# Kernel tuning notes

Measured on AMD Instinct MI355X. Metric: run time of the kernel, lower is better.

Reference implementation:

```python
import jax, jax.numpy as jnp
import numpy as np

DIM = 768
HQ = 8
HKV = 2
HD = 64
B = 1
S = 4096


def setup_inputs() -> dict:
    key = jax.random.key(0)
    ks = jax.random.split(key, 9)
    s = 0.02
    return {
        "x": jax.random.normal(ks[0], (B, S, DIM), jnp.float32),
        "Wq": jax.random.normal(ks[1], (DIM, HQ * HD), jnp.float32) * s,
        "bq": jax.random.normal(ks[2], (HQ * HD,), jnp.float32) * s,
        "Wk": jax.random.normal(ks[3], (DIM, HKV * HD), jnp.float32) * s,
        "bk": jax.random.normal(ks[4], (HKV * HD,), jnp.float32) * s,
        "Wv": jax.random.normal(ks[5], (DIM, HKV * HD), jnp.float32) * s,
        "bv": jax.random.normal(ks[6], (HKV * HD,), jnp.float32) * s,
        "Wo": jax.random.normal(ks[7], (HQ * HD, DIM), jnp.float32) * s,
        "bo": jax.random.normal(ks[8], (DIM,), jnp.float32) * s,
    }


def reference(x, Wq, bq, Wk, bk, Wv, bv, Wo, bo):
    bsz, q_len, _ = x.shape
    n_rep = HQ // HKV
    # projections
    q = (x @ Wq + bq).reshape(bsz, q_len, HQ, HD).transpose(0, 2, 1, 3)   # [b,hq,s,d]
    k = (x @ Wk + bk).reshape(bsz, q_len, HKV, HD).transpose(0, 2, 1, 3)  # [b,hkv,s,d]
    v = (x @ Wv + bv).reshape(bsz, q_len, HKV, HD).transpose(0, 2, 1, 3)
    # repeat_kv: expand kv heads to match query heads
    k = jnp.broadcast_to(k[:, :, None], (bsz, HKV, n_rep, q_len, HD)).reshape(bsz, HQ, q_len, HD)
    v = jnp.broadcast_to(v[:, :, None], (bsz, HKV, n_rep, q_len, HD)).reshape(bsz, HQ, q_len, HD)
    # full materialized attention (no mask in the original)
    att = jnp.einsum("bhqd,bhkd->bhqk", q, k) / jnp.sqrt(jnp.float32(HD))
    att = jax.nn.softmax(att.astype(jnp.float32), axis=-1).astype(q.dtype)  # [b,hq,s,s]
    out = jnp.einsum("bhqk,bhkd->bhqd", att, v)
    out = out.transpose(0, 2, 1, 3).reshape(bsz, q_len, HQ * HD)
    out = out @ Wo + bo
    return (out, att)
```

## Files before the change

### kernel.cpp

```cpp
#include <hip/hip_runtime.h>
#include <hip/hip_bf16.h>


#define DIM   768
#define Sc    4096

typedef __bf16 bfrag __attribute__((ext_vector_type(8)));
typedef float  facc  __attribute__((ext_vector_type(4)));

#define MFMA_BF16(a,b,c) __builtin_amdgcn_mfma_f32_16x16x32_bf16((a),(b),(c),0,0,0)

__global__ __launch_bounds__(256) void prep_kernel(
    const float* __restrict__ x,  const float* __restrict__ Wq,
    const float* __restrict__ Wk, const float* __restrict__ Wv,
    const float* __restrict__ Wo,
    __bf16* __restrict__ xb, __bf16* __restrict__ WqkvT, __bf16* __restrict__ WobT)
{
  int i = blockIdx.x * 256 + threadIdx.x;
  const int NX = Sc * DIM;
  const int NW = DIM * DIM;
  if (i < NX) { xb[i] = (__bf16)x[i]; return; }
  i -= NX;
  if (i < NW) {
    int n = i / DIM, c = i - n * DIM;
    float v;
    if (n < 512)      v = Wq[c * 512 + n];
    else if (n < 640) v = Wk[c * 128 + (n - 512)];
    else              v = Wv[c * 128 + (n - 640)];
    WqkvT[i] = (__bf16)v;
    return;
  }
  i -= NW;
  {
    int n = i / 512, k = i - n * 512;
    WobT[i] = (__bf16)Wo[k * DIM + n];
  }
}

template<int MODE>
__global__ __launch_bounds__(256) void gemm_kernel(
    const __bf16* __restrict__ A, const __bf16* __restrict__ BT, int Kd,
    const float* __restrict__ b0, const float* __restrict__ b1, const float* __restrict__ b2,
    __bf16* __restrict__ Qb, __bf16* __restrict__ Kb, __bf16* __restrict__ VTb,
    float* __restrict__ Cout)
{
  const int tid  = threadIdx.x;
  const int w    = tid >> 6;
  const int lane = tid & 63;
  const int i16  = lane & 15;
  const int quad = lane >> 4;
  const int n0   = blockIdx.x * 64;
  const int m0   = blockIdx.y * 64;

  __shared__ __attribute__((aligned(16))) __bf16 Al[64 * 72];
  __shared__ __attribute__((aligned(16))) __bf16 Bl[64 * 72];

  facc acc[4];
#pragma unroll
  for (int nt = 0; nt < 4; ++nt) acc[nt] = (facc){0.f, 0.f, 0.f, 0.f};

  const int nkt = Kd >> 6;
  for (int kt = 0; kt < nkt; ++kt) {
#pragma unroll
    for (int it = 0; it < 2; ++it) {
      int idx = tid + it * 256;
      int r = idx >> 3, ch = idx & 7;
      *(uint4*)&Al[r * 72 + ch * 8] =
          *(const uint4*)(A + (size_t)(m0 + r) * Kd + (kt * 64 + ch * 8));
    }
#pragma unroll
    for (int it = 0; it < 2; ++it) {
      int idx = tid + it * 256;
      int r = idx >> 3, ch = idx & 7;
      *(uint4*)&Bl[r * 72 + ch * 8] =
          *(const uint4*)(BT + (size_t)(n0 + r) * Kd + (kt * 64 + ch * 8));
    }
    __syncthreads();
#pragma unroll
    for (int ks = 0; ks < 2; ++ks) {
      bfrag a = *(const bfrag*)&Al[(w * 16 + i16) * 72 + ks * 32 + quad * 8];
#pragma unroll
      for (int nt = 0; nt < 4; ++nt) {
        bfrag b = *(const bfrag*)&Bl[(nt * 16 + i16) * 72 + ks * 32 + quad * 8];
        acc[nt] = MFMA_BF16(a, b, acc[nt]);
      }
    }
    __syncthreads();
  }

#pragma unroll
  for (int nt = 0; nt < 4; ++nt) {
    const int n = n0 + nt * 16 + i16;
    const int rbase = m0 + w * 16 + quad * 4;
    if (MODE == 0) {
      float bias;
      if (n < 512)      bias = b0[n];
      else if (n < 640) bias = b1[n - 512];
      else              bias = b2[n - 640];
#pragma unroll
      for (int reg = 0; reg < 4; ++reg) {
        float v = acc[nt][reg] + bias;
        int row = rbase + reg;
        if (n < 512) {
          int hh = n >> 6, d = n & 63;
          Qb[((size_t)hh * Sc + row) * 64 + d] = (__bf16)(v * 0.125f);
        } else if (n < 640) {
          int hh = (n - 512) >> 6, d = n & 63;
          Kb[((size_t)hh * Sc + row) * 64 + d] = (__bf16)v;
        } else {
          int hh = (n - 640) >> 6, d = n & 63;
          VTb[(size_t)hh * 64 * Sc + (size_t)d * Sc + row] = (__bf16)v;
        }
      }
    } else {
      float bias = b0[n];
#pragma unroll
      for (int reg = 0; reg < 4; ++reg)
        Cout[(size_t)(rbase + reg) * DIM + n] = acc[nt][reg] + bias;
    }
  }
}

#define PFSTRIDE 68
#define PFWAVE   (16 * PFSTRIDE + 4)

__global__ __launch_bounds__(256, 6) void attn_kernel(
    const __bf16* __restrict__ Qb, const __bf16* __restrict__ Kb,
    const __bf16* __restrict__ VTb,
    float* __restrict__ att, __bf16* __restrict__ OAb)
{
  const int tid  = threadIdx.x;
  const int w    = tid >> 6;
  const int lane = tid & 63;
  const int i16  = lane & 15;
  const int quad = lane >> 4;
  const int h    = blockIdx.y;
  const int kvh  = h >> 2;
  const int q0   = blockIdx.x * 16;

  __shared__ __attribute__((aligned(16))) float Pf[4 * PFWAVE];
  __shared__ float SM[4][16], SL[4][16];

  const __bf16* Kbase = Kb  + (size_t)kvh * Sc * 64;
  const __bf16* Vbase = VTb + (size_t)kvh * 64 * Sc;

  bfrag qf[2];
#pragma unroll
  for (int ks = 0; ks < 2; ++ks)
    qf[ks] = *(const bfrag*)(Qb + ((size_t)h * Sc + q0 + i16) * 64 + ks * 32 + quad * 8);

  float mrun[4], lrun[4];
#pragma unroll
  for (int r = 0; r < 4; ++r) { mrun[r] = -1e30f; lrun[r] = 0.f; }

  const int key0 = w * 1024;

  for (int kt = 0; kt < 16; ++kt) {
    const int kb0 = key0 + kt * 64;
    facc s[4];
#pragma unroll
    for (int nt = 0; nt < 4; ++nt) s[nt] = (facc){0.f, 0.f, 0.f, 0.f};
#pragma unroll
    for (int ks = 0; ks < 2; ++ks)
#pragma unroll
      for (int nt = 0; nt < 4; ++nt) {
        bfrag kf = *(const bfrag*)(Kbase + (size_t)(kb0 + nt * 16 + i16) * 64 + ks * 32 + quad * 8);
        s[nt] = MFMA_BF16(qf[ks], kf, s[nt]);
      }
#pragma unroll
    for (int r = 0; r < 4; ++r) {
      float tm = fmaxf(fmaxf(s[0][r], s[1][r]), fmaxf(s[2][r], s[3][r]));
      tm = fmaxf(tm, __shfl_xor(tm, 1));
      tm = fmaxf(tm, __shfl_xor(tm, 2));
      tm = fmaxf(tm, __shfl_xor(tm, 4));
      tm = fmaxf(tm, __shfl_xor(tm, 8));
      float mnew = fmaxf(mrun[r], tm);
      float ts = __expf(s[0][r] - mnew) + __expf(s[1][r] - mnew)
               + __expf(s[2][r] - mnew) + __expf(s[3][r] - mnew);
      ts += __shfl_xor(ts, 1);
      ts += __shfl_xor(ts, 2);
      ts += __shfl_xor(ts, 4);
      ts += __shfl_xor(ts, 8);
      lrun[r] = lrun[r] * __expf(mrun[r] - mnew) + ts;
      mrun[r] = mnew;
    }
  }

  if (i16 == 0) {
#pragma unroll
    for (int r = 0; r < 4; ++r) { SM[w][quad * 4 + r] = mrun[r]; SL[w][quad * 4 + r] = lrun[r]; }
  }
  __syncthreads();
  float mglob[4], linv[4];
#pragma unroll
  for (int r = 0; r < 4; ++r) {
    const int rr = quad * 4 + r;
    float m0v = SM[0][rr], m1v = SM[1][rr], m2v = SM[2][rr], m3v = SM[3][rr];
    float mg = fmaxf(fmaxf(m0v, m1v), fmaxf(m2v, m3v));
    float lg = SL[0][rr] * __expf(m0v - mg) + SL[1][rr] * __expf(m1v - mg)
             + SL[2][rr] * __expf(m2v - mg) + SL[3][rr] * __expf(m3v - mg);
    mglob[r] = mg;
    linv[r]  = 1.f / lg;
  }

  facc oacc[4];
#pragma unroll
  for (int nt = 0; nt < 4; ++nt) oacc[nt] = (facc){0.f, 0.f, 0.f, 0.f};

  float* attb = att + (size_t)h * Sc * Sc;
  float* Pw   = Pf + w * PFWAVE;

  for (int kt = 0; kt < 16; ++kt) {
    const int kb0 = key0 + kt * 64;
    facc s[4];
#pragma unroll
    for (int nt = 0; nt < 4; ++nt) s[nt] = (facc){0.f, 0.f, 0.f, 0.f};
#pragma unroll
    for (int ks = 0; ks < 2; ++ks)
#pragma unroll
      for (int nt = 0; nt < 4; ++nt) {
        bfrag kf = *(const bfrag*)(Kbase + (size_t)(kb0 + nt * 16 + i16) * 64 + ks * 32 + quad * 8);
        s[nt] = MFMA_BF16(qf[ks], kf, s[nt]);
      }
#pragma unroll
    for (int nt = 0; nt < 4; ++nt)
#pragma unroll
      for (int r = 0; r < 4; ++r)
        Pw[(quad * 4 + r) * PFSTRIDE + nt * 16 + i16] =
            __expf(s[nt][r] - mglob[r]) * linv[r];
    bfrag pa[2];
#pragma unroll
    for (int ks = 0; ks < 2; ++ks) {
      facc p0 = *(const facc*)&Pw[i16 * PFSTRIDE + ks * 32 + quad * 8];
      facc p1 = *(const facc*)&Pw[i16 * PFSTRIDE + ks * 32 + quad * 8 + 4];
      bfrag t;
      t[0] = (__bf16)p0[0]; t[1] = (__bf16)p0[1]; t[2] = (__bf16)p0[2]; t[3] = (__bf16)p0[3];
      t[4] = (__bf16)p1[0]; t[5] = (__bf16)p1[1]; t[6] = (__bf16)p1[2]; t[7] = (__bf16)p1[3];
      pa[ks] = t;
    }
#pragma unroll
    for (int ks = 0; ks < 2; ++ks)
#pragma unroll
      for (int nt = 0; nt < 4; ++nt) {
        bfrag vf = *(const bfrag*)(Vbase + (size_t)(nt * 16 + i16) * Sc + kb0 + ks * 32 + quad * 8);
        oacc[nt] = MFMA_BF16(pa[ks], vf, oacc[nt]);
      }
#pragma unroll
    for (int it = 0; it < 4; ++it) {
      int flat = it * 64 + lane;
      int row = flat >> 4, c4 = flat & 15;
      facc v = *(const facc*)&Pw[row * PFSTRIDE + c4 * 4];
      *(facc*)&attb[(size_t)(q0 + row) * Sc + kb0 + c4 * 4] = v;
    }
  }

#pragma unroll
  for (int nt = 0; nt < 4; ++nt)
#pragma unroll
    for (int r = 0; r < 4; ++r)
      Pw[(quad * 4 + r) * PFSTRIDE + nt * 16 + i16] = oacc[nt][r];
  __syncthreads();
#pragma unroll
  for (int it = 0; it < 4; ++it) {
    int e = it * 256 + tid;
    int row = e >> 6, d = e & 63;
    float sum = Pf[0 * PFWAVE + row * PFSTRIDE + d] + Pf[1 * PFWAVE + row * PFSTRIDE + d]
              + Pf[2 * PFWAVE + row * PFSTRIDE + d] + Pf[3 * PFWAVE + row * PFSTRIDE + d];
    OAb[(size_t)(q0 + row) * 512 + h * 64 + d] = (__bf16)sum;
  }
}

extern "C" void kernel_launch(void* const* d_in, const int* in_sizes, int n_in,
                              void* d_out, int out_size, void* d_ws, size_t ws_size,
                              hipStream_t stream) {
  const float* x  = (const float*)d_in[0];
  const float* Wq = (const float*)d_in[1];
  const float* bq = (const float*)d_in[2];
  const float* Wk = (const float*)d_in[3];
  const float* bk = (const float*)d_in[4];
  const float* Wv = (const float*)d_in[5];
  const float* bv = (const float*)d_in[6];
  const float* Wo = (const float*)d_in[7];
  const float* bo = (const float*)d_in[8];

  float* out = (float*)d_out;
  float* att = out + (size_t)Sc * DIM;

  char* ws = (char*)d_ws;
  size_t off = 0;
  __bf16* xb    = (__bf16*)(ws + off); off += (size_t)Sc * DIM * 2;
  __bf16* WqkvT = (__bf16*)(ws + off); off += (size_t)DIM * DIM * 2;
  __bf16* WobT  = (__bf16*)(ws + off); off += (size_t)DIM * 512 * 2;
  __bf16* Qb    = (__bf16*)(ws + off); off += (size_t)8 * Sc * 64 * 2;
  __bf16* Kb    = (__bf16*)(ws + off); off += (size_t)2 * Sc * 64 * 2;
  __bf16* VTb   = (__bf16*)(ws + off); off += (size_t)2 * 64 * Sc * 2;
  __bf16* OAb   = (__bf16*)(ws + off); off += (size_t)Sc * 512 * 2;

  prep_kernel<<<16128, 256, 0, stream>>>(x, Wq, Wk, Wv, Wo, xb, WqkvT, WobT);
  gemm_kernel<0><<<dim3(12, 64), 256, 0, stream>>>(xb, WqkvT, 768, bq, bk, bv,
                                                   Qb, Kb, VTb, nullptr);
  attn_kernel<<<dim3(256, 8), 256, 0, stream>>>(Qb, Kb, VTb, att, OAb);
  gemm_kernel<1><<<dim3(12, 64), 256, 0, stream>>>(OAb, WobT, 512, bo, nullptr, nullptr,
                                                   nullptr, nullptr, nullptr, out);
}
```

Measured before the change: 876.7 us.

## Use exp2 softmax with folded log2e scale, lazy row reductions, V prefetch and nontemporal stores

Result: slower. 995.8 us (+13.6%).

```diff
diff --git a/kernel.cpp b/kernel.cpp
--- a/kernel.cpp
+++ b/kernel.cpp
@@ -4,6 +4,7 @@
 
 #define DIM   768
 #define Sc    4096
+#define QSCALE 0.180336880111120419f
 
 typedef __bf16 bfrag __attribute__((ext_vector_type(8)));
 typedef float  facc  __attribute__((ext_vector_type(4)));
@@ -103,7 +104,7 @@
         int row = rbase + reg;
         if (n < 512) {
           int hh = n >> 6, d = n & 63;
-          Qb[((size_t)hh * Sc + row) * 64 + d] = (__bf16)(v * 0.125f);
+          Qb[((size_t)hh * Sc + row) * 64 + d] = (__bf16)(v * QSCALE);
         } else if (n < 640) {
           int hh = (n - 512) >> 6, d = n & 63;
           Kb[((size_t)hh * Sc + row) * 64 + d] = (__bf16)v;
@@ -149,17 +150,18 @@
   for (int ks = 0; ks < 2; ++ks)
     qf[ks] = *(const bfrag*)(Qb + ((size_t)h * Sc + q0 + i16) * 64 + ks * 32 + quad * 8);
 
+  const int key0 = w * 1024;
+
   float mrun[4], lrun[4];
 #pragma unroll
   for (int r = 0; r < 4; ++r) { mrun[r] = -1e30f; lrun[r] = 0.f; }
-
-  const int key0 = w * 1024;
 
   for (int kt = 0; kt < 16; ++kt) {
     const int kb0 = key0 + kt * 64;
     facc s[4];
 #pragma unroll
     for (int nt = 0; nt < 4; ++nt) s[nt] = (facc){0.f, 0.f, 0.f, 0.f};
+    __builtin_amdgcn_s_setprio(1);
 #pragma unroll
     for (int ks = 0; ks < 2; ++ks)
 #pragma unroll
@@ -167,38 +169,43 @@
         bfrag kf = *(const bfrag*)(Kbase + (size_t)(kb0 + nt * 16 + i16) * 64 + ks * 32 + quad * 8);
         s[nt] = MFMA_BF16(qf[ks], kf, s[nt]);
       }
+    __builtin_amdgcn_s_setprio(0);
 #pragma unroll
     for (int r = 0; r < 4; ++r) {
-      float tm = fmaxf(fmaxf(s[0][r], s[1][r]), fmaxf(s[2][r], s[3][r]));
-      tm = fmaxf(tm, __shfl_xor(tm, 1));
-      tm = fmaxf(tm, __shfl_xor(tm, 2));
-      tm = fmaxf(tm, __shfl_xor(tm, 4));
-      tm = fmaxf(tm, __shfl_xor(tm, 8));
+      float t0 = s[0][r], t1 = s[1][r], t2 = s[2][r], t3 = s[3][r];
+      float tm   = fmaxf(fmaxf(t0, t1), fmaxf(t2, t3));
       float mnew = fmaxf(mrun[r], tm);
-      float ts = __expf(s[0][r] - mnew) + __expf(s[1][r] - mnew)
-               + __expf(s[2][r] - mnew) + __expf(s[3][r] - mnew);
-      ts += __shfl_xor(ts, 1);
-      ts += __shfl_xor(ts, 2);
-      ts += __shfl_xor(ts, 4);
-      ts += __shfl_xor(ts, 8);
-      lrun[r] = lrun[r] * __expf(mrun[r] - mnew) + ts;
+      float ts = exp2f(t0 - mnew) + exp2f(t1 - mnew)
+               + exp2f(t2 - mnew) + exp2f(t3 - mnew);
+      lrun[r] = lrun[r] * exp2f(mrun[r] - mnew) + ts;
       mrun[r] = mnew;
     }
   }
 
-  if (i16 == 0) {
-#pragma unroll
-    for (int r = 0; r < 4; ++r) { SM[w][quad * 4 + r] = mrun[r]; SL[w][quad * 4 + r] = lrun[r]; }
+#pragma unroll
+  for (int r = 0; r < 4; ++r) {
+    float m = mrun[r];
+    m = fmaxf(m, __shfl_xor(m, 1));
+    m = fmaxf(m, __shfl_xor(m, 2));
+    m = fmaxf(m, __shfl_xor(m, 4));
+    m = fmaxf(m, __shfl_xor(m, 8));
+    float l = lrun[r] * exp2f(mrun[r] - m);
+    l += __shfl_xor(l, 1);
+    l += __shfl_xor(l, 2);
+    l += __shfl_xor(l, 4);
+    l += __shfl_xor(l, 8);
+    if (i16 == 0) { SM[w][quad * 4 + r] = m; SL[w][quad * 4 + r] = l; }
   }
   __syncthreads();
+
   float mglob[4], linv[4];
 #pragma unroll
   for (int r = 0; r < 4; ++r) {
     const int rr = quad * 4 + r;
     float m0v = SM[0][rr], m1v = SM[1][rr], m2v = SM[2][rr], m3v = SM[3][rr];
     float mg = fmaxf(fmaxf(m0v, m1v), fmaxf(m2v, m3v));
-    float lg = SL[0][rr] * __expf(m0v - mg) + SL[1][rr] * __expf(m1v - mg)
-             + SL[2][rr] * __expf(m2v - mg) + SL[3][rr] * __expf(m3v - mg);
+    float lg = SL[0][rr] * exp2f(m0v - mg) + SL[1][rr] * exp2f(m1v - mg)
+             + SL[2][rr] * exp2f(m2v - mg) + SL[3][rr] * exp2f(m3v - mg);
     mglob[r] = mg;
     linv[r]  = 1.f / lg;
   }
@@ -215,6 +222,7 @@
     facc s[4];
 #pragma unroll
     for (int nt = 0; nt < 4; ++nt) s[nt] = (facc){0.f, 0.f, 0.f, 0.f};
+    __builtin_amdgcn_s_setprio(1);
 #pragma unroll
     for (int ks = 0; ks < 2; ++ks)
 #pragma unroll
@@ -222,12 +230,25 @@
         bfrag kf = *(const bfrag*)(Kbase + (size_t)(kb0 + nt * 16 + i16) * 64 + ks * 32 + quad * 8);
         s[nt] = MFMA_BF16(qf[ks], kf, s[nt]);
       }
+    __builtin_amdgcn_s_setprio(0);
+
+    bfrag vf0[4];
+#pragma unroll
+    for (int nt = 0; nt < 4; ++nt)
+      vf0[nt] = *(const bfrag*)(Vbase + (size_t)(nt * 16 + i16) * Sc + kb0 + quad * 8);
+
 #pragma unroll
     for (int nt = 0; nt < 4; ++nt)
 #pragma unroll
       for (int r = 0; r < 4; ++r)
         Pw[(quad * 4 + r) * PFSTRIDE + nt * 16 + i16] =
-            __expf(s[nt][r] - mglob[r]) * linv[r];
+            exp2f(s[nt][r] - mglob[r]) * linv[r];
+
+    bfrag vf1[4];
+#pragma unroll
+    for (int nt = 0; nt < 4; ++nt)
+      vf1[nt] = *(const bfrag*)(Vbase + (size_t)(nt * 16 + i16) * Sc + kb0 + 32 + quad * 8);
+
     bfrag pa[2];
 #pragma unroll
     for (int ks = 0; ks < 2; ++ks) {
@@ -238,19 +259,20 @@
       t[4] = (__bf16)p1[0]; t[5] = (__bf16)p1[1]; t[6] = (__bf16)p1[2]; t[7] = (__bf16)p1[3];
       pa[ks] = t;
     }
-#pragma unroll
-    for (int ks = 0; ks < 2; ++ks)
-#pragma unroll
-      for (int nt = 0; nt < 4; ++nt) {
-        bfrag vf = *(const bfrag*)(Vbase + (size_t)(nt * 16 + i16) * Sc + kb0 + ks * 32 + quad * 8);
-        oacc[nt] = MFMA_BF16(pa[ks], vf, oacc[nt]);
-      }
+
+    __builtin_amdgcn_s_setprio(1);
+#pragma unroll
+    for (int nt = 0; nt < 4; ++nt) oacc[nt] = MFMA_BF16(pa[0], vf0[nt], oacc[nt]);
+#pragma unroll
+    for (int nt = 0; nt < 4; ++nt) oacc[nt] = MFMA_BF16(pa[1], vf1[nt], oacc[nt]);
+    __builtin_amdgcn_s_setprio(0);
+
 #pragma unroll
     for (int it = 0; it < 4; ++it) {
       int flat = it * 64 + lane;
       int row = flat >> 4, c4 = flat & 15;
       facc v = *(const facc*)&Pw[row * PFSTRIDE + c4 * 4];
-      *(facc*)&attb[(size_t)(q0 + row) * Sc + kb0 + c4 * 4] = v;
+      __builtin_nontemporal_store(v, (facc*)&attb[(size_t)(q0 + row) * Sc + kb0 + c4 * 4]);
     }
   }
 
```
